# Performance work log

Hardware: AMD Instinct MI355X
Metric: run time of the kernel (lower is better)

## Reference

```python
import jax, jax.numpy as jnp
import numpy as np

B, N_PER, K = 8, 4096, 16          # graphs, nodes per graph, knn neighbors
D_IN, D_H, D_OUT = 32, 64, 128     # feature_nn: 35->64->64, global_nn: 64->128
N = B * N_PER


def setup_inputs() -> dict:
    key = jax.random.key(0)
    ks = jax.random.split(key, 8)
    sc = lambda fan: 1.0 / np.sqrt(fan)
    x = jax.random.normal(ks[0], (N, D_IN), jnp.float32)
    pos = jax.random.normal(ks[1], (N, 3), jnp.float32)
    batch = jnp.repeat(jnp.arange(B, dtype=jnp.int32), N_PER)
    fW1 = jax.random.normal(ks[2], (D_IN + 3, D_H), jnp.float32) * sc(D_IN + 3)
    fb1 = jnp.zeros((D_H,), jnp.float32)
    fW2 = jax.random.normal(ks[3], (D_H, D_H), jnp.float32) * sc(D_H)
    fb2 = jnp.zeros((D_H,), jnp.float32)
    gW = jax.random.normal(ks[4], (D_H, D_OUT), jnp.float32) * sc(D_H)
    gb = jnp.zeros((D_OUT,), jnp.float32)
    return {"x": x, "pos": pos, "batch": batch,
            "fW1": fW1, "fb1": fb1, "fW2": fW2, "fb2": fb2,
            "gW": gW, "gb": gb}


def reference(x, pos, batch, fW1, fb1, fW2, fb2, gW, gb):
    # ---- knn(pos, pos, k, batch, batch): per-graph k nearest (self included) ----
    posb = pos.reshape(B, N_PER, 3)
    sq = jnp.sum(posb * posb, axis=-1)                      # [B, Nper]
    dist = sq[:, :, None] + sq[:, None, :] - 2.0 * jnp.einsum('bnd,bmd->bnm', posb, posb)
    _, nbr = jax.lax.top_k(-dist, K)                        # [B, Nper, K] local neighbor idx
    offs = (jnp.arange(B, dtype=nbr.dtype) * N_PER)[:, None, None]
    col = (nbr + offs).reshape(-1)                          # edge_index[1]: neighbor (x) idx
    row = jnp.repeat(jnp.arange(N, dtype=col.dtype), K)     # edge_index[0]: query (y) idx

    # ---- PointConv: msg = feature_nn(cat[x_j, pos_j - pos_i]), max-aggregate at i ----
    # PyG flow source_to_target: j = edge_index[0] = row (query), i = edge_index[1] = col.
    msg = jnp.concatenate([x[row], pos[row] - pos[col]], axis=1)  # [E, 35]
    h = jax.nn.relu(msg @ fW1 + fb1)
    h = jax.nn.relu(h @ fW2 + fb2)                          # [E, 64]
    agg = jax.ops.segment_max(h, col, num_segments=N)       # max aggregation
    agg = jnp.where(jnp.isfinite(agg), agg, 0.0)            # PyG fills empty segments with 0
    out = jax.nn.relu(agg @ gW + gb)                        # global_nn
    return (out, pos, batch)
```

## Files before the change

### kernel.cpp

```cpp
#include <hip/hip_runtime.h>
#include <hip/hip_bf16.h>

#define N_PER    4096
#define KNBR     16
#define NTOT     32768
#define D_IN     32
#define D_H      64
#define D_OUT    128
#define E_TOT    (NTOT * KNBR)

#define OUT1_OFF (NTOT * D_OUT)
#define OUT2_OFF (NTOT * D_OUT + NTOT*3)

#define KNN_INF 3.4e38f

typedef __attribute__((ext_vector_type(8))) short bf16x8;
typedef __attribute__((ext_vector_type(4))) float f32x4;

__device__ float          g_posf[NTOT * 3];
__device__ float          g_scf[NTOT];
__device__ int            g_nbr[E_TOT];
__device__ unsigned short g_base1h[NTOT * D_H];
__device__ uint4          g_Bfrag[2 * 4 * 64];
__device__ float          g_Wd[3 * D_H];
__device__ float          g_fb2v[D_H];
__device__ int            g_cnt[NTOT];
__device__ int            g_bsum[NTOT / 256];
__device__ int            g_offs[NTOT + 1];
__device__ int            g_cursor[NTOT];
__device__ int            g_inlist[E_TOT];
__device__ float          g_agg[NTOT * D_H];

__device__ __forceinline__ float ldf(const void* p, int i, int bf) {
    if (bf) return __uint_as_float(((unsigned)((const unsigned short*)p)[i]) << 16);
    return ((const float*)p)[i];
}
__device__ __forceinline__ unsigned bf16rne(float f) {
    unsigned u = __float_as_uint(f);
    return (u + 0x7FFFu + ((u >> 16) & 1u)) >> 16;
}
__device__ __forceinline__ void stf(void* p, int i, float v, int bf) {
    if (bf) ((unsigned short*)p)[i] = (unsigned short)bf16rne(v);
    else    ((float*)p)[i] = v;
}
__device__ __forceinline__ float b2f(unsigned short h) {
    return __uint_as_float(((unsigned)h) << 16);
}
__device__ __forceinline__ int wave_probe(const void* x) {
    unsigned wv = ((const unsigned*)x)[threadIdx.x & 63];
    unsigned e = (wv >> 7) & 0xFFu;
    unsigned long long mk = __ballot(e >= 110u && e <= 140u);
    return (__popcll(mk) >= 32) ? 1 : 0;
}

__global__ __launch_bounds__(256) void prep_kernel(const void* __restrict__ x,
                                                   const void* __restrict__ pos,
                                                   const void* __restrict__ fW1,
                                                   const void* __restrict__ fb1,
                                                   const void* __restrict__ fW2,
                                                   const void* __restrict__ fb2) {
    const int bf = wave_probe(x);
    const int b = blockIdx.x;
    if (b < 1024) {
        const int i0 = b * 256 + threadIdx.x;
        const int stride = 1024 * 256;
        for (int i = i0; i < NTOT * 3; i += stride) g_posf[i] = ldf(pos, i, bf);
        {
#pragma clang fp contract(off)
            for (int i = i0; i < NTOT; i += stride) {
                float a = ldf(pos, i * 3 + 0, bf);
                float c2 = ldf(pos, i * 3 + 1, bf);
                float c3 = ldf(pos, i * 3 + 2, bf);
                g_scf[i] = a * a + c2 * c2 + c3 * c3;
                g_cnt[i] = 0;
            }
        }
        for (int i = i0; i < NTOT * D_H; i += stride) g_agg[i] = 0.0f;
    } else if (b < 2048) {
        int lane = threadIdx.x & 63, wid = threadIdx.x >> 6;
        int n0 = (b - 1024) * 32 + wid * 8;
        float wcol[D_IN];
#pragma unroll
        for (int k = 0; k < D_IN; k++) wcol[k] = ldf(fW1, k * D_H + lane, bf);
        float bb = ldf(fb1, lane, bf);
        for (int r = 0; r < 8; r++) {
            int n = n0 + r;
            float acc = bb;
#pragma unroll
            for (int k = 0; k < D_IN; k++) acc += ldf(x, n * D_IN + k, bf) * wcol[k];
            g_base1h[(size_t)n * D_H + lane] = (unsigned short)bf16rne(acc);
        }
    } else {
        for (int t = threadIdx.x; t < 3 * D_H; t += 256) g_Wd[t] = ldf(fW1, D_IN * D_H + t, bf);
        if (threadIdx.x < D_H) g_fb2v[threadIdx.x] = ldf(fb2, threadIdx.x, bf);
        for (int idx = threadIdx.x; idx < 512; idx += 256) {
            int lane = idx & 63, nt = (idx >> 6) & 3, ks = idx >> 8;
            int n = nt * 16 + (lane & 15);
            int k0 = ks * 32 + ((lane >> 4) << 3);
            unsigned wds[4];
#pragma unroll
            for (int jp = 0; jp < 4; jp++) {
                unsigned lo = bf16rne(ldf(fW2, (k0 + 2 * jp) * D_H + n, bf));
                unsigned hi = bf16rne(ldf(fW2, (k0 + 2 * jp + 1) * D_H + n, bf));
                wds[jp] = lo | (hi << 16);
            }
            g_Bfrag[idx] = make_uint4(wds[0], wds[1], wds[2], wds[3]);
        }
    }
}

__global__ __launch_bounds__(256) void knn_kernel() {
#pragma clang fp contract(off)
    __shared__ int s_i[4][8][64];
    const int lane = threadIdx.x & 63;
    const int wid  = threadIdx.x >> 6;
    const int qbase = blockIdx.x * 32 + wid * 8;
    const int cbase = (qbase >> 12) << 12;
    const float* cp  = g_posf + cbase * 3;
    const float* csc = g_scf + cbase;

    float qx[8], qy[8], qz[8], qs[8];
#pragma unroll
    for (int r = 0; r < 8; r++) {
        qx[r] = g_posf[(qbase + r) * 3 + 0];
        qy[r] = g_posf[(qbase + r) * 3 + 1];
        qz[r] = g_posf[(qbase + r) * 3 + 2];
        qs[r] = g_scf[qbase + r];
    }

    float m[8];
#pragma unroll
    for (int r = 0; r < 8; r++) m[r] = KNN_INF;
    for (int c = 0; c < 64; c++) {
        int jj = c * 64 + lane;
        float px = cp[jj * 3], py = cp[jj * 3 + 1], pz = cp[jj * 3 + 2];
        float sc = csc[jj];
#pragma unroll
        for (int r = 0; r < 8; r++) {
            float dot = fmaf(pz, qz[r], fmaf(py, qy[r], px * qx[r]));
            float d = fmaf(-2.0f, dot, qs[r] + sc);
            m[r] = fminf(m[r], d);
        }
    }

    float T[8];
#pragma unroll
    for (int r = 0; r < 8; r++) {
        float v = m[r];
#pragma unroll
        for (int k = 2; k <= 64; k <<= 1) {
#pragma unroll
            for (int j2 = k >> 1; j2 >= 1; j2 >>= 1) {
                float pv = __shfl_xor(v, j2);
                bool keepMin = (((lane & j2) == 0) == ((lane & k) == 0));
                bool tp = ((pv < v) == keepMin);
                v = tp ? pv : v;
            }
        }
        T[r] = __shfl(v, 15) + 1e-3f;
    }

    int cnt[8];
#pragma unroll
    for (int r = 0; r < 8; r++) cnt[r] = 0;
    for (int c = 0; c < 64; c++) {
        int jj = c * 64 + lane;
        float px = cp[jj * 3], py = cp[jj * 3 + 1], pz = cp[jj * 3 + 2];
        float sc = csc[jj];
#pragma unroll
        for (int r = 0; r < 8; r++) {
            float dot = fmaf(pz, qz[r], fmaf(py, qy[r], px * qx[r]));
            float d = fmaf(-2.0f, dot, qs[r] + sc);
            bool p = (d <= T[r]);
            unsigned long long mk = __ballot(p);
            if (mk) {
                int pre = (int)__popcll(mk & ((1ull << lane) - 1ull));
                int slot = cnt[r] + pre;
                if (p && slot < 64) s_i[wid][r][slot] = cbase + jj;
                cnt[r] += (int)__popcll(mk);
            }
        }
    }
    __syncthreads();

#pragma unroll
    for (int r = 0; r < 8; r++) {
        int q = qbase + r;
        if (cnt[r] <= 64) {
            int S = cnt[r];
            int idx = (lane < S) ? s_i[wid][r][lane] : 0x7FFFFFFF;
            float d = KNN_INF;
            if (lane < S) {
                float px = g_posf[idx * 3], py = g_posf[idx * 3 + 1], pz = g_posf[idx * 3 + 2];
                float sc = g_scf[idx];
                float dot = px * qx[r] + py * qy[r] + pz * qz[r];
                d = (qs[r] + sc) - 2.0f * dot;
            }
#pragma unroll
            for (int k = 2; k <= 64; k <<= 1) {
#pragma unroll
                for (int j2 = k >> 1; j2 >= 1; j2 >>= 1) {
                    float pd = __shfl_xor(d, j2);
                    int   pi = __shfl_xor(idx, j2);
                    bool keepMin = (((lane & j2) == 0) == ((lane & k) == 0));
                    bool lt = (pd < d) || (pd == d && pi < idx);
                    bool tp = (lt == keepMin);
                    d   = tp ? pd : d;
                    idx = tp ? pi : idx;
                }
            }
            if (lane < 16) {
                g_nbr[q * KNBR + lane] = idx;
                atomicAdd(&g_cnt[idx & (NTOT - 1)], 1);
            }
        } else {
            float lastd = -KNN_INF; int lasti = -1;
            for (int t = 0; t < 16; t++) {
                float bd = KNN_INF; int bi = 0x7FFFFFFF;
                for (int c = 0; c < 64; c++) {
                    int jj = c * 64 + lane;
                    float px = cp[jj * 3], py = cp[jj * 3 + 1], pz = cp[jj * 3 + 2];
                    float sc = csc[jj];
                    float dot = px * qx[r] + py * qy[r] + pz * qz[r];
                    float dd = (qs[r] + sc) - 2.0f * dot;
                    int gj = cbase + jj;
                    bool after  = (dd > lastd) || (dd == lastd && gj > lasti);
                    bool better = (dd < bd) || (dd == bd && gj < bi);
                    if (after && better) { bd = dd; bi = gj; }
                }
#pragma unroll
                for (int s2 = 1; s2 < 64; s2 <<= 1) {
                    float od = __shfl_xor(bd, s2);
                    int   oi = __shfl_xor(bi, s2);
                    if (od < bd || (od == bd && oi < bi)) { bd = od; bi = oi; }
                }
                if (lane == 0) {
                    g_nbr[q * KNBR + t] = bi;
                    atomicAdd(&g_cnt[bi & (NTOT - 1)], 1);
                }
                lastd = bd; lasti = bi;
            }
        }
    }
}

__global__ __launch_bounds__(256) void scanA_kernel() {
    __shared__ int red[4];
    int t = threadIdx.x, lane = t & 63, w = t >> 6;
    int v = g_cnt[blockIdx.x * 256 + t];
    int s = v;
#pragma unroll
    for (int off = 1; off < 64; off <<= 1) s += __shfl_xor(s, off);
    if (lane == 0) red[w] = s;
    __syncthreads();
    if (t == 0) g_bsum[blockIdx.x] = red[0] + red[1] + red[2] + red[3];
}

__global__ __launch_bounds__(256) void scanC_kernel() {
    __shared__ int sred[4];
    __shared__ int wsum[4];
    int t = threadIdx.x, lane = t & 63, w = t >> 6;
    int contrib = (t < 128 && t < blockIdx.x) ? g_bsum[t] : 0;
    int rs = contrib;
#pragma unroll
    for (int off = 1; off < 64; off <<= 1) rs += __shfl_xor(rs, off);
    if (lane == 0) sred[w] = rs;
    __syncthreads();
    int base = sred[0] + sred[1] + sred[2] + sred[3];

    int i = blockIdx.x * 256 + t;
    int v = g_cnt[i];
    int inc = v;
#pragma unroll
    for (int off = 1; off < 64; off <<= 1) {
        int u = __shfl_up(inc, off);
        if (lane >= off) inc += u;
    }
    if (lane == 63) wsum[w] = inc;
    __syncthreads();
    int wbase = 0;
    for (int k = 0; k < w; k++) wbase += wsum[k];
    int excl = base + wbase + inc - v;
    g_offs[i] = excl;
    g_cursor[i] = excl;
    if (i == NTOT - 1) g_offs[NTOT] = E_TOT;
}

__global__ void scatter_kernel() {
    int e = blockIdx.x * 256 + threadIdx.x;
    int c = g_nbr[e] & (NTOT - 1);
    int slot = atomicAdd(&g_cursor[c], 1);
    g_inlist[slot & (E_TOT - 1)] = e;
}

__global__ __launch_bounds__(256) void edge_kernel() {
    __shared__ unsigned short sA[256 * 72];
    __shared__ int scol[256];
    const int t    = threadIdx.x;
    const int lane = t & 63;
    const int w    = t >> 6;
    const int slot0 = blockIdx.x * 256;

    {
        int e = g_inlist[slot0 + t];
        int n = (e >> 4) & (NTOT - 1);
        int j = g_nbr[e] & (NTOT - 1);
        scol[t] = j;
        float dx = g_posf[n * 3 + 0] - g_posf[j * 3 + 0];
        float dy = g_posf[n * 3 + 1] - g_posf[j * 3 + 1];
        float dz = g_posf[n * 3 + 2] - g_posf[j * 3 + 2];
        const unsigned short* b1 = g_base1h + (size_t)n * D_H;
#pragma unroll
        for (int d0 = 0; d0 < D_H; d0 += 8) {
            uint4 p = *(const uint4*)(b1 + d0);
            unsigned pw[4] = {p.x, p.y, p.z, p.w};
            unsigned qw[4];
#pragma unroll
            for (int jp = 0; jp < 4; jp++) {
                int d = d0 + 2 * jp;
                float v0 = __uint_as_float(pw[jp] << 16)
                         + dx * g_Wd[d]     + dy * g_Wd[64 + d]     + dz * g_Wd[128 + d];
                float v1 = __uint_as_float(pw[jp] & 0xFFFF0000u)
                         + dx * g_Wd[d + 1] + dy * g_Wd[64 + d + 1] + dz * g_Wd[128 + d + 1];
                v0 = fmaxf(v0, 0.f); v1 = fmaxf(v1, 0.f);
                qw[jp] = bf16rne(v0) | (bf16rne(v1) << 16);
            }
            *(uint4*)(&sA[t * 72 + d0]) = make_uint4(qw[0], qw[1], qw[2], qw[3]);
        }
    }
    __syncthreads();

    f32x4 acc[4][4];
#pragma unroll
    for (int a = 0; a < 4; a++)
#pragma unroll
        for (int b = 0; b < 4; b++) acc[a][b] = (f32x4){0.f, 0.f, 0.f, 0.f};

    const int quad = lane >> 4;
    const int l15  = lane & 15;
#pragma unroll
    for (int ks = 0; ks < 2; ks++) {
        bf16x8 bfrag[4];
#pragma unroll
        for (int nt = 0; nt < 4; nt++)
            bfrag[nt] = ((const bf16x8*)g_Bfrag)[ks * 256 + nt * 64 + lane];
#pragma unroll
        for (int mt = 0; mt < 4; mt++) {
            int row = w * 64 + mt * 16 + l15;
            bf16x8 afrag = *(const bf16x8*)(&sA[row * 72 + ks * 32 + quad * 8]);
#pragma unroll
            for (int nt = 0; nt < 4; nt++)
                acc[mt][nt] = __builtin_amdgcn_mfma_f32_16x16x32_bf16(afrag, bfrag[nt], acc[mt][nt], 0, 0, 0);
        }
    }
    __syncthreads();

#pragma unroll
    for (int nt = 0; nt < 4; nt++) {
        int dim = nt * 16 + l15;
        float bb = g_fb2v[dim];
#pragma unroll
        for (int mt = 0; mt < 4; mt++) {
#pragma unroll
            for (int r = 0; r < 4; r++) {
                int edge = w * 64 + mt * 16 + quad * 4 + r;
                float v = fmaxf(acc[mt][nt][r] + bb, 0.f);
                sA[edge * 72 + dim] = (unsigned short)bf16rne(v);
            }
        }
    }
    __syncthreads();

    {
        const int ls0 = w * 64;
        const int gs0 = slot0 + ls0;
        int cur = -1;
        float vmax = 0.f;
        for (int s = ls0; s < ls0 + 64; s++) {
            int cj = scol[s];
            float v = b2f(sA[s * 72 + lane]);
            if (cj != cur) {
                if (cur >= 0) {
                    int lo = g_offs[cur], hi = g_offs[cur + 1];
                    if (lo >= gs0 && hi <= gs0 + 64)
                        g_agg[(size_t)cur * D_H + lane] = vmax;
                    else
                        atomicMax((unsigned*)&g_agg[(size_t)cur * D_H + lane], __float_as_uint(vmax));
                }
                cur = cj; vmax = v;
            } else {
                vmax = fmaxf(vmax, v);
            }
        }
        if (cur >= 0) {
            int lo = g_offs[cur], hi = g_offs[cur + 1];
            if (lo >= gs0 && hi <= gs0 + 64)
                g_agg[(size_t)cur * D_H + lane] = vmax;
            else
                atomicMax((unsigned*)&g_agg[(size_t)cur * D_H + lane], __float_as_uint(vmax));
        }
    }
}

__global__ __launch_bounds__(256) void outmisc_kernel(const void* __restrict__ x,
                                                      const void* __restrict__ gW,
                                                      const void* __restrict__ gb,
                                                      const int* __restrict__ batch,
                                                      const void* __restrict__ pos,
                                                      void* __restrict__ out) {
    const int bf = wave_probe(x);
    const int b = blockIdx.x;
    if (b < 2048) {
        int t = threadIdx.x, d = t & 127, half = t >> 7;
        float gcol[D_H];
#pragma unroll
        for (int k = 0; k < D_H; k++) gcol[k] = ldf(gW, k * D_OUT + d, bf);
        float bb = ldf(gb, d, bf);
        int n0 = b * 16 + half * 8;
        for (int r = 0; r < 8; r++) {
            int n = n0 + r;
            float acc = bb;
#pragma unroll
            for (int k = 0; k < D_H; k++) acc += g_agg[(size_t)n * D_H + k] * gcol[k];
            stf(out, n * D_OUT + d, fmaxf(acc, 0.f), bf);
        }
    } else {
        int i = (b - 2048) * 256 + threadIdx.x;
        if (bf) {
            if (i < NTOT * 3) ((unsigned short*)out)[OUT1_OFF + i] = ((const unsigned short*)pos)[i];
            if (i < NTOT)     ((unsigned short*)out)[OUT2_OFF + i] = (unsigned short)bf16rne((float)batch[i]);
        } else {
            if (i < NTOT * 3) ((float*)out)[OUT1_OFF + i] = ((const float*)pos)[i];
            if (i < NTOT)     ((float*)out)[OUT2_OFF + i] = (float)batch[i];
        }
    }
}

extern "C" void kernel_launch(void* const* d_in, const int* in_sizes, int n_in,
                              void* d_out, int out_size, void* d_ws, size_t ws_size,
                              hipStream_t stream) {
    const void* x     = d_in[0];
    const void* pos   = d_in[1];
    const int*  batch = (const int*)d_in[2];
    const void* fW1   = d_in[3];
    const void* fb1   = d_in[4];
    const void* fW2   = d_in[5];
    const void* fb2   = d_in[6];
    const void* gW    = d_in[7];
    const void* gb    = d_in[8];

    hipLaunchKernelGGL(prep_kernel,    dim3(2049),        dim3(256), 0, stream, x, pos, fW1, fb1, fW2, fb2);
    hipLaunchKernelGGL(knn_kernel,     dim3(NTOT / 32),   dim3(256), 0, stream);
    hipLaunchKernelGGL(scanA_kernel,   dim3(NTOT / 256),  dim3(256), 0, stream);
    hipLaunchKernelGGL(scanC_kernel,   dim3(NTOT / 256),  dim3(256), 0, stream);
    hipLaunchKernelGGL(scatter_kernel, dim3(E_TOT / 256), dim3(256), 0, stream);
    hipLaunchKernelGGL(edge_kernel,    dim3(E_TOT / 256), dim3(256), 0, stream);
    hipLaunchKernelGGL(outmisc_kernel, dim3(2048 + (NTOT * 3 + 255) / 256), dim3(256), 0, stream,
                       x, gW, gb, batch, pos, d_out);
}
```

Measured before the change: 294.9 us.

## Stage KNN candidate positions in shared memory and vectorize x loads in prep

The KNN kernel now uses 512-thread blocks that cooperatively stage 1024-point chunks of candidate positions and squared norms into LDS, in SoA form, for both the min pass and the threshold/ballot pass. This replaces per-wave strided global loads with shared reads. The prep kernel's base layer-1 projection loads each x row with 128-bit vector loads, in both the bf16 and fp32 paths. The cost is extra block-wide barriers per chunk and higher LDS use per block, which may limit occupancy.

```diff
diff --git a/kernel.cpp b/kernel.cpp
--- a/kernel.cpp
+++ b/kernel.cpp
@@ -83,12 +83,39 @@
 #pragma unroll
         for (int k = 0; k < D_IN; k++) wcol[k] = ldf(fW1, k * D_H + lane, bf);
         float bb = ldf(fb1, lane, bf);
-        for (int r = 0; r < 8; r++) {
-            int n = n0 + r;
-            float acc = bb;
-#pragma unroll
-            for (int k = 0; k < D_IN; k++) acc += ldf(x, n * D_IN + k, bf) * wcol[k];
-            g_base1h[(size_t)n * D_H + lane] = (unsigned short)bf16rne(acc);
+        if (bf) {
+            const unsigned short* xp = (const unsigned short*)x;
+            for (int r = 0; r < 8; r++) {
+                int n = n0 + r;
+                const uint4* xr = (const uint4*)(xp + (size_t)n * D_IN);
+                float acc = bb;
+#pragma unroll
+                for (int q4 = 0; q4 < 4; q4++) {
+                    uint4 w4 = xr[q4];
+                    unsigned ww[4] = {w4.x, w4.y, w4.z, w4.w};
+#pragma unroll
+                    for (int p = 0; p < 4; p++) {
+                        int k = q4 * 8 + p * 2;
+                        acc += __uint_as_float(ww[p] << 16) * wcol[k];
+                        acc += __uint_as_float(ww[p] & 0xFFFF0000u) * wcol[k + 1];
+                    }
+                }
+                g_base1h[(size_t)n * D_H + lane] = (unsigned short)bf16rne(acc);
+            }
+        } else {
+            const float* xp = (const float*)x;
+            for (int r = 0; r < 8; r++) {
+                int n = n0 + r;
+                const float4* xr = (const float4*)(xp + (size_t)n * D_IN);
+                float acc = bb;
+#pragma unroll
+                for (int q4 = 0; q4 < 8; q4++) {
+                    float4 w4 = xr[q4];
+                    int k = q4 * 4;
+                    acc += w4.x * wcol[k] + w4.y * wcol[k + 1] + w4.z * wcol[k + 2] + w4.w * wcol[k + 3];
+                }
+                g_base1h[(size_t)n * D_H + lane] = (unsigned short)bf16rne(acc);
+            }
         }
     } else {
         for (int t = threadIdx.x; t < 3 * D_H; t += 256) g_Wd[t] = ldf(fW1, D_IN * D_H + t, bf);
@@ -109,12 +136,13 @@
     }
 }
 
-__global__ __launch_bounds__(256) void knn_kernel() {
+__global__ __launch_bounds__(512) void knn_kernel() {
 #pragma clang fp contract(off)
-    __shared__ int s_i[4][8][64];
+    __shared__ float s_px[1024], s_py[1024], s_pz[1024], s_sc[1024];
+    __shared__ int s_i[8][8][64];
     const int lane = threadIdx.x & 63;
     const int wid  = threadIdx.x >> 6;
-    const int qbase = blockIdx.x * 32 + wid * 8;
+    const int qbase = blockIdx.x * 64 + wid * 8;
     const int cbase = (qbase >> 12) << 12;
     const float* cp  = g_posf + cbase * 3;
     const float* csc = g_scf + cbase;
@@ -131,15 +159,26 @@
     float m[8];
 #pragma unroll
     for (int r = 0; r < 8; r++) m[r] = KNN_INF;
-    for (int c = 0; c < 64; c++) {
-        int jj = c * 64 + lane;
-        float px = cp[jj * 3], py = cp[jj * 3 + 1], pz = cp[jj * 3 + 2];
-        float sc = csc[jj];
-#pragma unroll
-        for (int r = 0; r < 8; r++) {
-            float dot = fmaf(pz, qz[r], fmaf(py, qy[r], px * qx[r]));
-            float d = fmaf(-2.0f, dot, qs[r] + sc);
-            m[r] = fminf(m[r], d);
+    for (int ch = 0; ch < 4; ch++) {
+        __syncthreads();
+        const float* gp = cp + ch * 1024 * 3;
+        for (int i = threadIdx.x; i < 1024; i += 512) {
+            s_px[i] = gp[i * 3 + 0];
+            s_py[i] = gp[i * 3 + 1];
+            s_pz[i] = gp[i * 3 + 2];
+            s_sc[i] = csc[ch * 1024 + i];
+        }
+        __syncthreads();
+#pragma unroll 4
+        for (int c = 0; c < 16; c++) {
+            int jj = c * 64 + lane;
+            float px = s_px[jj], py = s_py[jj], pz = s_pz[jj], sc = s_sc[jj];
+#pragma unroll
+            for (int r = 0; r < 8; r++) {
+                float dot = fmaf(pz, qz[r], fmaf(py, qy[r], px * qx[r]));
+                float d = fmaf(-2.0f, dot, qs[r] + sc);
+                m[r] = fminf(m[r], d);
+            }
         }
     }
 
@@ -163,25 +202,34 @@
     int cnt[8];
 #pragma unroll
     for (int r = 0; r < 8; r++) cnt[r] = 0;
-    for (int c = 0; c < 64; c++) {
-        int jj = c * 64 + lane;
-        float px = cp[jj * 3], py = cp[jj * 3 + 1], pz = cp[jj * 3 + 2];
-        float sc = csc[jj];
-#pragma unroll
-        for (int r = 0; r < 8; r++) {
-            float dot = fmaf(pz, qz[r], fmaf(py, qy[r], px * qx[r]));
-            float d = fmaf(-2.0f, dot, qs[r] + sc);
-            bool p = (d <= T[r]);
-            unsigned long long mk = __ballot(p);
-            if (mk) {
-                int pre = (int)__popcll(mk & ((1ull << lane) - 1ull));
-                int slot = cnt[r] + pre;
-                if (p && slot < 64) s_i[wid][r][slot] = cbase + jj;
-                cnt[r] += (int)__popcll(mk);
-            }
-        }
-    }
-    __syncthreads();
+    for (int ch = 0; ch < 4; ch++) {
+        __syncthreads();
+        const float* gp = cp + ch * 1024 * 3;
+        for (int i = threadIdx.x; i < 1024; i += 512) {
+            s_px[i] = gp[i * 3 + 0];
+            s_py[i] = gp[i * 3 + 1];
+            s_pz[i] = gp[i * 3 + 2];
+            s_sc[i] = csc[ch * 1024 + i];
+        }
+        __syncthreads();
+        for (int c = 0; c < 16; c++) {
+            int jj = c * 64 + lane;
+            float px = s_px[jj], py = s_py[jj], pz = s_pz[jj], sc = s_sc[jj];
+#pragma unroll
+            for (int r = 0; r < 8; r++) {
+                float dot = fmaf(pz, qz[r], fmaf(py, qy[r], px * qx[r]));
+                float d = fmaf(-2.0f, dot, qs[r] + sc);
+                bool p = (d <= T[r]);
+                unsigned long long mk = __ballot(p);
+                if (mk) {
+                    int pre = (int)__popcll(mk & ((1ull << lane) - 1ull));
+                    int slot = cnt[r] + pre;
+                    if (p && slot < 64) s_i[wid][r][slot] = cbase + ch * 1024 + jj;
+                    cnt[r] += (int)__popcll(mk);
+                }
+            }
+        }
+    }
 
 #pragma unroll
     for (int r = 0; r < 8; r++) {
@@ -450,7 +498,7 @@
     const void* gb    = d_in[8];
 
     hipLaunchKernelGGL(prep_kernel,    dim3(2049),        dim3(256), 0, stream, x, pos, fW1, fb1, fW2, fb2);
-    hipLaunchKernelGGL(knn_kernel,     dim3(NTOT / 32),   dim3(256), 0, stream);
+    hipLaunchKernelGGL(knn_kernel,     dim3(NTOT / 64),   dim3(512), 0, stream);
     hipLaunchKernelGGL(scanA_kernel,   dim3(NTOT / 256),  dim3(256), 0, stream);
     hipLaunchKernelGGL(scanC_kernel,   dim3(NTOT / 256),  dim3(256), 0, stream);
     hipLaunchKernelGGL(scatter_kernel, dim3(E_TOT / 256), dim3(256), 0, stream);
```

New measurement: 276.2 us. -6.4%, faster.
